# Kernel tuning notes

Hardware: AMD Instinct MI355X
Metric: run time of the kernel (lower is better)

The kernel has to match this reference:

```python
import jax, jax.numpy as jnp
import numpy as np

DIM, DFF, NH = 768, 2048, 12
HD = DIM // NH
N, NOBJ, L = 16, 52, 24
EPS = 1e-5


def setup_inputs() -> dict:
    key = jax.random.key(0)
    ks = jax.random.split(key, 16)
    g = lambda k, shape: jax.random.normal(k, shape, jnp.float32) * 0.02
    inp = {
        "lang": jax.random.normal(ks[0], (N, L, DIM), jnp.float32),
        "obj": jax.random.normal(ks[1], (N, NOBJ, DIM), jnp.float32),
        "lang_mask": jnp.ones((N, L), jnp.int32),
        "obj_mask": jnp.ones((N, NOBJ), jnp.int32),
        "co_mask": jnp.ones((N, L, NOBJ), jnp.int32),
    }
    # two multi-head attention blocks (edge / node): q,k,v,o projections
    for i, nm in enumerate(["e_wq", "e_wk", "e_wv", "e_wo", "n_wq", "n_wk", "n_wv", "n_wo"]):
        inp[nm] = g(ks[2 + i], (DIM, DIM))
        inp[nm.replace("w", "b")] = jnp.zeros((DIM,), jnp.float32)
    inp["ffn_w1"] = g(ks[10], (2 * DIM, DFF)); inp["ffn_b1"] = jnp.zeros((DFF,), jnp.float32)
    inp["ffn_w2"] = g(ks[11], (DFF, DIM)); inp["ffn_b2"] = jnp.zeros((DIM,), jnp.float32)
    for nm in ["ln_e", "ln_q", "ln2"]:
        inp[nm + "_g"] = jnp.ones((DIM,), jnp.float32)
        inp[nm + "_b"] = jnp.zeros((DIM,), jnp.float32)
    return inp


def _layernorm(x, g, b):
    m = jnp.mean(x, -1, keepdims=True)
    v = jnp.mean((x - m) ** 2, -1, keepdims=True)
    return (x - m) * jax.lax.rsqrt(v + EPS) * g + b


def _fwd(lang, obj, co_mask,
         e_wq, e_bq, e_wk, e_bk, e_wv, e_bv, e_wo, e_bo,
         n_wq, n_bq, n_wk, n_bk, n_wv, n_bv, n_wo, n_bo,
         ffn_w1, ffn_b1, ffn_w2, ffn_b2,
         ln_e_g, ln_e_b, ln_q_g, ln_q_b, ln2_g, ln2_b):
    scale = jnp.float32(1.0 / np.sqrt(HD))
    co_t = co_mask.swapaxes(1, 2)  # [N, nobj, L]: query objects attend over lang keys

    # ---- node branch: standard cross-attention obj -> lang ----
    qh = (obj @ n_wq + n_bq).reshape(N, NOBJ, NH, HD)
    kh = (lang @ n_wk + n_bk).reshape(N, L, NH, HD)
    vh = (lang @ n_wv + n_bv).reshape(N, L, NH, HD)
    s = jnp.einsum('nqhd,nlhd->nhql', qh, kh) * scale  # [N,H,nobj,L]
    s = jnp.where(co_t[:, None, :, :] > 0, s, jnp.float32(-1e9))
    a = jax.nn.softmax(s, axis=-1)
    node = jnp.einsum('nhql,nlhd->nqhd', a, vh).reshape(N, NOBJ, DIM) @ n_wo + n_bo

    # ---- edge branch: pairwise diffs attend over lang, then max over partner ----
    diff = obj[:, :, None, :] - obj[:, None, :, :]            # [N,i,j,D]
    qhe = (diff @ e_wq + e_bq).reshape(N, NOBJ, NOBJ, NH, HD)
    khe = (lang @ e_wk + e_bk).reshape(N, L, NH, HD)
    vhe = (lang @ e_wv + e_bv).reshape(N, L, NH, HD)
    se = jnp.einsum('nijhd,nlhd->nhijl', qhe, khe) * scale    # [N,H,i,j,L]
    # mask depends on (n, j, l): torch repeats co_mask^T over the i batch dim
    se = jnp.where(co_t[:, None, None, :, :] > 0, se, jnp.float32(-1e9))
    ae = jax.nn.softmax(se, axis=-1)
    oe = jnp.einsum('nhijl,nlhd->nijhd', ae, vhe).reshape(N, NOBJ, NOBJ, DIM)
    oe = oe @ e_wo + e_bo                                      # [N,i,j,D]
    edge = jnp.max(oe, axis=2)                                 # max over query/partner j -> [N,i,D]

    # ---- fuse ----
    xe = _layernorm(obj + edge, ln_e_g, ln_e_b)
    xn = _layernorm(obj + node, ln_q_g, ln_q_b)
    h = jnp.concatenate((xn, xe), -1)
    h = jax.nn.relu(h @ ffn_w1 + ffn_b1) @ ffn_w2 + ffn_b2
    return _layernorm(xn + h, ln2_g, ln2_b)


def reference(lang, obj, lang_mask, obj_mask, co_mask,
              e_wq, e_bq, e_wk, e_bk, e_wv, e_bv, e_wo, e_bo,
              n_wq, n_bq, n_wk, n_bk, n_wv, n_bv, n_wo, n_bo,
              ffn_w1, ffn_b1, ffn_w2, ffn_b2,
              ln_e_g, ln_e_b, ln_q_g, ln_q_b, ln2_g, ln2_b):
    return _fwd(lang, obj, co_mask,
                e_wq, e_bq, e_wk, e_bk, e_wv, e_bv, e_wo, e_bo,
                n_wq, n_bq, n_wk, n_bk, n_wv, n_bv, n_wo, n_bo,
                ffn_w1, ffn_b1, ffn_w2, ffn_b2,
                ln_e_g, ln_e_b, ln_q_g, ln_q_b, ln2_g, ln2_b)
```

## Files before the change

kernel.cpp:

```cpp
#include <hip/hip_runtime.h>
#include <math.h>

#define NOBJ 52
#define LL 24
#define NHEAD 12

typedef __attribute__((ext_vector_type(8))) short bf16x8;
typedef __attribute__((ext_vector_type(4))) float f32x4;
typedef __attribute__((ext_vector_type(4))) unsigned int u32x4;
typedef __attribute__((ext_vector_type(2))) unsigned int u32x2;

__device__ __forceinline__ unsigned short f2b(float x) {
    union { float f; unsigned int u; } v; v.f = x;
    unsigned int r = v.u + 0x7fffu + ((v.u >> 16) & 1u);
    return (unsigned short)(r >> 16);
}
__device__ __forceinline__ float b2f(unsigned short u) {
    union { unsigned int u; float f; } v; v.u = ((unsigned int)u) << 16;
    return v.f;
}
__device__ __forceinline__ unsigned int pack2(float a, float b) {
    return (unsigned int)f2b(a) | ((unsigned int)f2b(b) << 16);
}
__device__ __forceinline__ f32x4 mfma16(bf16x8 a, bf16x8 b, f32x4 c) {
    return __builtin_amdgcn_mfma_f32_16x16x32_bf16(a, b, c, 0, 0, 0);
}
__device__ __forceinline__ void gl_lds16(const void* g, void* lds) {
    __builtin_amdgcn_global_load_lds(
        (const __attribute__((address_space(1))) unsigned int*)g,
        (__attribute__((address_space(3))) unsigned int*)lds, 16, 0, 0);
}

__device__ __forceinline__ void transpose_tile(const float* __restrict__ src,
    unsigned short* __restrict__ dst, int K, int N, int t, char* smem)
{
    float (*ts)[65] = (float(*)[65])smem;
    const int tid = threadIdx.x;
    const int ntk = K >> 6;
    const int k0 = (t % ntk) << 6, n0 = (t / ntk) << 6;
    const int tx = tid & 63, ty = tid >> 6;
    #pragma unroll
    for (int i2 = 0; i2 < 16; ++i2) {
        const int row = i2 * 4 + ty;
        ts[row][tx] = src[(size_t)(k0 + row) * N + n0 + tx];
    }
    __syncthreads();
    #pragma unroll
    for (int i2 = 0; i2 < 16; ++i2) {
        const int row = i2 * 4 + ty;
        dst[(size_t)(n0 + row) * K + k0 + tx] = f2b(ts[tx][row]);
    }
}

__global__ __launch_bounds__(256)
void pack1_kernel(const float* s0, const float* s1, const float* s2,
                  const float* s3, const float* s4, const float* s5,
                  const float* s6, const float* s7,
                  unsigned short* d0, unsigned short* d1, unsigned short* d2,
                  unsigned short* d3, unsigned short* d4, unsigned short* d5,
                  unsigned short* d6, unsigned short* d7,
                  const float* obj, const float* lang, const float* n_bq,
                  const float* e_bk, const float* e_bv,
                  const float* n_bk, const float* n_bv,
                  unsigned short* objb, unsigned short* langb,
                  float* bqc, float* blc)
{
    __shared__ __align__(16) char smem[16640];
    const int bid = blockIdx.x;
    const int tid = threadIdx.x;
    if (bid < 1152) {
        const int job = bid / 144, t = bid % 144;
        const float* src; unsigned short* dst;
        switch (job) {
            case 0: src = s0; dst = d0; break;
            case 1: src = s1; dst = d1; break;
            case 2: src = s2; dst = d2; break;
            case 3: src = s3; dst = d3; break;
            case 4: src = s4; dst = d4; break;
            case 5: src = s5; dst = d5; break;
            case 6: src = s6; dst = d6; break;
            default: src = s7; dst = d7; break;
        }
        transpose_tile(src, dst, 768, 768, t, smem);
    } else {
        const int base = ((bid - 1152) * 256 + tid) * 4;
        const int T0 = 638976, T1 = 933888, T2 = 935424, T3 = 938496;
        if (base >= T3) return;
        if (base < T0) {
            f32x4 v = *(const f32x4*)(obj + base);
            *(u32x2*)(objb + base) = (u32x2){pack2(v[0], v[1]), pack2(v[2], v[3])};
        } else if (base < T1) {
            const int j = base - T0;
            f32x4 v = *(const f32x4*)(lang + j);
            *(u32x2*)(langb + j) = (u32x2){pack2(v[0], v[1]), pack2(v[2], v[3])};
        } else if (base < T2) {
            const int j = base - T1;
            if (j < 768) { *(f32x4*)(bqc + j) = (f32x4){0.f, 0.f, 0.f, 0.f}; }
            else         { *(f32x4*)(bqc + j) = *(const f32x4*)(n_bq + j - 768); }
        } else {
            const int j = base - T2;
            const int s = j / 768, c = j % 768;
            const float* p = (s == 0) ? e_bk : (s == 1) ? e_bv : (s == 2) ? n_bk : n_bv;
            *(f32x4*)(blc + j) = *(const f32x4*)(p + c);
        }
    }
}

struct GemmJob {
    const unsigned short* A; const unsigned short* Bt; const float* bias;
    float* C; unsigned short* Cb;
    int lda, ldb, ldc, K, nbx, nb, relu, swz;
};

__device__ __forceinline__ void gemm_body(const GemmJob J, int bid, char* smem)
{
    unsigned short* As = (unsigned short*)smem;
    unsigned short* Bs = (unsigned short*)(smem + 16384);
    int bx, by;
    if (J.swz) {
        const int cpx = J.nb >> 3;
        const int gid = (bid & 7) * cpx + (bid >> 3);
        const int nbm = J.nb / J.nbx;
        bx = gid / nbm; by = gid % nbm;
    } else { bx = bid % J.nbx; by = bid / J.nbx; }
    const int n0 = bx * 128, m0 = by * 64;
    const int tid = threadIdx.x;
    const int lane = tid & 63;
    const int w = tid >> 6, wr = w >> 1, wc = w & 1;
    const int lr = lane & 15, lk = lane >> 4;
    const int lda = J.lda, ldb = J.ldb, K = J.K;
    const unsigned short* Ab = J.A + (size_t)m0 * lda;
    const unsigned short* Bb = J.Bt + (size_t)n0 * ldb;

    f32x4 acc[2][4] = {};
    const int NT = K >> 6;

    #pragma unroll
    for (int q = 0; q < 2; ++q) {
        const int c = q * 256 + tid, row = c >> 3, p = (c & 7) ^ (row & 7);
        gl_lds16(Ab + (size_t)row * lda + p * 8, As + c * 8);
    }
    #pragma unroll
    for (int q = 0; q < 4; ++q) {
        const int c = q * 256 + tid, row = c >> 3, p = (c & 7) ^ (row & 7);
        gl_lds16(Bb + (size_t)row * ldb + p * 8, Bs + c * 8);
    }
    __syncthreads();

    for (int t = 0; t < NT; ++t) {
        const int cur = t & 1;
        if (t + 1 < NT) {
            const int k0 = (t + 1) << 6;
            #pragma unroll
            for (int q = 0; q < 2; ++q) {
                const int c = q * 256 + tid, row = c >> 3, p = (c & 7) ^ (row & 7);
                gl_lds16(Ab + (size_t)row * lda + k0 + p * 8, As + (cur ^ 1) * 4096 + c * 8);
            }
            #pragma unroll
            for (int q = 0; q < 4; ++q) {
                const int c = q * 256 + tid, row = c >> 3, p = (c & 7) ^ (row & 7);
                gl_lds16(Bb + (size_t)row * ldb + k0 + p * 8, Bs + (cur ^ 1) * 8192 + c * 8);
            }
        }
        #pragma unroll
        for (int kk = 0; kk < 2; ++kk) {
            bf16x8 af[2], bv[4];
            #pragma unroll
            for (int mt = 0; mt < 2; ++mt) {
                const int row = wr * 32 + mt * 16 + lr;
                const int pc = (kk * 4 + lk) ^ (row & 7);
                af[mt] = *(const bf16x8*)(As + cur * 4096 + row * 64 + pc * 8);
            }
            #pragma unroll
            for (int nt = 0; nt < 4; ++nt) {
                const int col = wc * 64 + nt * 16 + lr;
                const int pc = (kk * 4 + lk) ^ (col & 7);
                bv[nt] = *(const bf16x8*)(Bs + cur * 8192 + col * 64 + pc * 8);
            }
            #pragma unroll
            for (int mt = 0; mt < 2; ++mt)
                #pragma unroll
                for (int nt = 0; nt < 4; ++nt)
                    acc[mt][nt] = mfma16(af[mt], bv[nt], acc[mt][nt]);
        }
        __syncthreads();
    }

    #pragma unroll
    for (int mt = 0; mt < 2; ++mt) {
        #pragma unroll
        for (int nt = 0; nt < 4; ++nt) {
            const int col = n0 + wc * 64 + nt * 16 + lr;
            const float bvv = J.bias ? J.bias[col] : 0.f;
            #pragma unroll
            for (int r = 0; r < 4; ++r) {
                const int row = m0 + wr * 32 + mt * 16 + lk * 4 + r;
                float v = acc[mt][nt][r] + bvv;
                if (J.relu) v = fmaxf(v, 0.f);
                if (J.C)  J.C[(size_t)row * J.ldc + col] = v;
                if (J.Cb) J.Cb[(size_t)row * J.ldc + col] = f2b(v);
            }
        }
    }
}

__global__ __launch_bounds__(256)
void gemm_tn4(GemmJob j0, GemmJob j1, GemmJob j2, GemmJob j3)
{
    __shared__ __align__(16) char smem[49152];
    int bid = blockIdx.x;
    if (bid < j0.nb) { gemm_body(j0, bid, smem); return; }
    bid -= j0.nb;
    if (bid < j1.nb) { gemm_body(j1, bid, smem); return; }
    bid -= j1.nb;
    if (bid < j2.nb) { gemm_body(j2, bid, smem); return; }
    bid -= j2.nb;
    gemm_body(j3, bid, smem);
}

__global__ __launch_bounds__(256)
void proj_pack_kernel(GemmJob j0, GemmJob j1,
                      const float* w1, const float* w2,
                      unsigned short* W1t, unsigned short* W2t)
{
    __shared__ __align__(16) char smem[49152];
    int bid = blockIdx.x;
    if (bid < j0.nb) { gemm_body(j0, bid, smem); return; }
    bid -= j0.nb;
    if (bid < j1.nb) { gemm_body(j1, bid, smem); return; }
    const int t = bid - j1.nb;
    if (t < 768) transpose_tile(w1, W1t, 1536, 2048, t, smem);
    else transpose_tile(w2, W2t, 2048, 768, t - 768, smem);
}

__global__ __launch_bounds__(256)
void mid3_kernel(const unsigned short* __restrict__ QCb,
                 const unsigned short* __restrict__ LCb,
                 const unsigned short* __restrict__ Wet,
                 const unsigned short* __restrict__ Wot,
                 const float* __restrict__ e_bq,
                 unsigned short* __restrict__ VWe,
                 unsigned short* __restrict__ VWn,
                 float* __restrict__ S2e, float* __restrict__ Tb,
                 float* __restrict__ S2n)
{
    __shared__ __align__(16) union USm {
        struct { unsigned short As[8192], Bs[8192]; } g;
        unsigned short Ct[128 * 136];
        struct { float sA[52][65], sB[24][65]; } s;
    } U;
    const int bid = blockIdx.x;
    const int tid = threadIdx.x;

    if (bid < 432) {
        const int sub = bid >= 216;
        const int b = sub ? bid - 216 : bid;
        const int aoff = sub ? 2304 : 768;
        const unsigned short* Bt = sub ? Wot : Wet;
        unsigned short* Vout = sub ? VWn : VWe;

        const int h = b / 18, rm = b % 18, mt = rm / 6, ntile = rm % 6;
        const int m0 = mt * 128, n0 = ntile * 128;
        const int lane = tid & 63, w = tid >> 6, wr = w >> 1, wc = w & 1;
        const int lr = lane & 15, lk = lane >> 4;
        #pragma unroll
        for (int q = 0; q < 4; ++q) {
            const int c = q * 256 + tid, row = c >> 3, p = (c & 7) ^ (row & 7);
            gl_lds16(LCb + (size_t)(m0 + row) * 3072 + aoff + h * 64 + p * 8, &U.g.As[c * 8]);
            gl_lds16(Bt + (size_t)(n0 + row) * 768 + h * 64 + p * 8, &U.g.Bs[c * 8]);
        }
        __syncthreads();
        f32x4 acc[4][4] = {};
        #pragma unroll
        for (int kk = 0; kk < 2; ++kk) {
            bf16x8 af[4], bv[4];
            #pragma unroll
            for (int m2 = 0; m2 < 4; ++m2) {
                const int row = wr * 64 + m2 * 16 + lr;
                const int pc = (kk * 4 + lk) ^ (row & 7);
                af[m2] = *(const bf16x8*)&U.g.As[row * 64 + pc * 8];
            }
            #pragma unroll
            for (int n2 = 0; n2 < 4; ++n2) {
                const int col = wc * 64 + n2 * 16 + lr;
                const int pc = (kk * 4 + lk) ^ (col & 7);
                bv[n2] = *(const bf16x8*)&U.g.Bs[col * 64 + pc * 8];
            }
            #pragma unroll
            for (int m2 = 0; m2 < 4; ++m2)
                #pragma unroll
                for (int n2 = 0; n2 < 4; ++n2)
                    acc[m2][n2] = mfma16(af[m2], bv[n2], acc[m2][n2]);
        }
        __syncthreads();
        #pragma unroll
        for (int m2 = 0; m2 < 4; ++m2)
            #pragma unroll
            for (int n2 = 0; n2 < 4; ++n2) {
                const int col = wc * 64 + n2 * 16 + lr;
                #pragma unroll
                for (int r = 0; r < 4; ++r) {
                    const int row = wr * 64 + m2 * 16 + lk * 4 + r;
                    U.Ct[row * 136 + col] = f2b(acc[m2][n2][r]);
                }
            }
        __syncthreads();
        #pragma unroll
        for (int q = 0; q < 8; ++q) {
            const int item = q * 256 + tid;
            const int dl = item & 127, kg = item >> 7;
            const int m = m0 + kg * 8;
            const int nn = m / 24, l0 = m % 24;
            const int kc = (h * 24 + l0) >> 3;
            const int ks = kc >> 2;
            const int dg = n0 + dl;
            const int kpos = (kc & 3) ^ ((dg >> 1) & 3);
            u32x4 uu;
            #pragma unroll
            for (int e = 0; e < 4; ++e)
                uu[e] = (unsigned int)U.Ct[(kg * 8 + 2 * e) * 136 + dl]
                      | ((unsigned int)U.Ct[(kg * 8 + 2 * e + 1) * 136 + dl] << 16);
            *(u32x4*)(Vout + (size_t)nn * 221184 + ks * 24576 + dg * 32 + kpos * 8) = uu;
        }
    } else {
        const int sub = bid >= 624;
        const int b = bid - (sub ? 624 : 432);
        const int n = b / NHEAD, h = b % NHEAD;
        const int qoff = sub ? 768 : 0, koff = sub ? 1536 : 0;
        float* Sout = sub ? S2n : S2e;
        for (int p = tid; p < 52 * 64; p += 256) {
            const int q = p >> 6, d = p & 63;
            U.s.sA[q][d] = b2f(QCb[(size_t)(n * 52 + q) * 1536 + qoff + h * 64 + d]);
        }
        for (int p = tid; p < 24 * 64; p += 256) {
            const int l = p >> 6, d = p & 63;
            U.s.sB[l][d] = b2f(LCb[(size_t)(n * 24 + l) * 3072 + koff + h * 64 + d]);
        }
        __syncthreads();
        for (int p = tid; p < 52 * 24; p += 256) {
            const int l = p / 52, q = p % 52;
            float s = 0.f;
            #pragma unroll
            for (int d = 0; d < 64; ++d) s += U.s.sA[q][d] * U.s.sB[l][d];
            Sout[((size_t)(n * NHEAD + h) * 24 + l) * 52 + q] = s;
        }
        if (!sub && tid < 24) {
            float s = 0.f;
            #pragma unroll
            for (int d = 0; d < 64; ++d) s += e_bq[h * 64 + d] * U.s.sB[tid][d];
            Tb[((size_t)n * NHEAD + h) * 24 + tid] = s;
        }
    }
}

__global__ __launch_bounds__(512)
void attn_kernel(const float* __restrict__ S2e, const float* __restrict__ Tb,
                 const float* __restrict__ S2n, const int* __restrict__ co_mask,
                 const unsigned short* __restrict__ VWe,
                 const unsigned short* __restrict__ VWn,
                 const float* __restrict__ ebo, const float* __restrict__ nbo,
                 unsigned short* __restrict__ EdgeBb,
                 unsigned short* __restrict__ NodePb)
{
    __shared__ __align__(16) char smem[126464];
    unsigned short* Pf = (unsigned short*)smem;
    unsigned short* Bs = (unsigned short*)(smem + 73728);
    float* SiT = (float*)(smem + 122880);
    unsigned char* cmb = (unsigned char*)(smem + 125184);
    const int bid = blockIdx.x;
    const int tid = threadIdx.x;
    const int lane = tid & 63, w = tid >> 6;
    const int lr = lane & 15, lk = lane >> 4;

    if (bid < 832) {
        const int sw = (bid & 7) * 104 + (bid >> 3);
        const int n = sw / 52;
        const int r52 = sw % 52;
        const int ip = r52 >> 1, dh = r52 & 1;
        const int i0 = ip * 2;
        const unsigned short* Bsrc = VWe + (size_t)n * 221184 + dh * 12288;
        const float* S2x = S2e + (size_t)n * NHEAD * 24 * 52;

        #pragma unroll
        for (int q = 0; q < 3; ++q) {
            const int c = q * 512 + tid;
            gl_lds16(Bsrc + c * 8, Bs + c * 8);
        }
        for (int p = tid; p < 576; p += 512) {
            const int ii = p >= 288 ? 1 : 0;
            const int rl = p - ii * 288;
            SiT[ii * 288 + rl] = S2x[(size_t)rl * 52 + i0 + ii]
                               + Tb[(size_t)n * 288 + rl];
        }
        for (int p = tid; p < 1248; p += 512)
            cmb[p] = (unsigned char)(co_mask[(size_t)n * 1248 + p] > 0);
        __syncthreads();

        for (int p = tid; p < 1248; p += 512) {
            const int ii = p >= 624 ? 1 : 0;
            const int rl = p - ii * 624;
            const int h = rl / 52, j = rl % 52;
            const float* Sc = S2x + (size_t)h * 1248 + j;
            const float* st = SiT + ii * 288 + h * 24;
            float x[24]; float mx = -1e30f;
            #pragma unroll
            for (int l = 0; l < 24; ++l) {
                float v = (st[l] - Sc[l * 52]) * 0.125f;
                v = cmb[l * 52 + j] ? v : -1e9f;
                x[l] = v; mx = fmaxf(mx, v);
            }
            float sum = 0.f;
            #pragma unroll
            for (int l = 0; l < 24; ++l) { const float e = __expf(x[l] - mx); x[l] = e; sum += e; }
            const float inv = 1.f / sum;
            unsigned short* Prow = Pf + ii * 18432 + j * 288;
            const int swk = (j >> 1) & 3;
            #pragma unroll
            for (int c = 0; c < 3; ++c) {
                u32x4 u;
                #pragma unroll
                for (int m = 0; m < 4; ++m)
                    u[m] = pack2(x[c * 8 + 2 * m] * inv, x[c * 8 + 2 * m + 1] * inv);
                *(u32x4*)(Prow + (((3 * h + c) ^ swk) << 3)) = u;
            }
        }
        __syncthreads();

        const int iw = w >> 2, cg = (w & 3) * 96;
        f32x4 acc[4][6] = {};
        for (int ks = 0; ks < 9; ++ks) {
            const int cur = ks & 1;
            if (ks < 8) {
                const unsigned short* src = Bsrc + (size_t)(ks + 1) * 24576;
                #pragma unroll
                for (int q = 0; q < 3; ++q) {
                    const int c = q * 512 + tid;
                    gl_lds16(src + c * 8, Bs + (cur ^ 1) * 12288 + c * 8);
                }
            }
            bf16x8 af[4];
            #pragma unroll
            for (int mt = 0; mt < 4; ++mt) {
                const int row = mt * 16 + lr;
                af[mt] = *(const bf16x8*)(Pf + iw * 18432 + row * 288
                                          + (((ks * 4 + lk) ^ ((row >> 1) & 3)) << 3));
            }
            #pragma unroll
            for (int nt = 0; nt < 6; ++nt) {
                const int cl = cg + nt * 16 + lr;
                bf16x8 bv = *(const bf16x8*)(Bs + cur * 12288 + cl * 32
                                             + ((lk ^ ((cl >> 1) & 3)) << 3));
                #pragma unroll
                for (int mt = 0; mt < 4; ++mt)
                    acc[mt][nt] = mfma16(af[mt], bv, acc[mt][nt]);
            }
            __syncthreads();
        }

        #pragma unroll
        for (int nt = 0; nt < 6; ++nt) {
            float m = -1e30f;
            #pragma unroll
            for (int mt = 0; mt < 4; ++mt)
                #pragma unroll
                for (int r = 0; r < 4; ++r) {
                    const int row = mt * 16 + lk * 4 + r;
                    if (row < NOBJ) m = fmaxf(m, acc[mt][nt][r]);
                }
            m = fmaxf(m, __shfl_xor(m, 16));
            m = fmaxf(m, __shfl_xor(m, 32));
            if (lk == 0) {
                const int col = dh * 384 + cg + nt * 16 + lr;
                EdgeBb[(size_t)(n * 52 + i0 + iw) * 768 + col] = f2b(m + ebo[col]);
            }
        }
    } else {
        const int t = bid - 832;
        const int n = t >> 1, dh = t & 1;
        const unsigned short* Bsrc = VWn + (size_t)n * 221184 + dh * 12288;
        const float* S2x = S2n + (size_t)n * NHEAD * 24 * 52;

        #pragma unroll
        for (int q = 0; q < 3; ++q) {
            const int c = q * 512 + tid;
            gl_lds16(Bsrc + c * 8, Bs + c * 8);
        }
        for (int p = tid; p < 1248; p += 512)
            cmb[p] = (unsigned char)(co_mask[(size_t)n * 1248 + p] > 0);
        __syncthreads();

        for (int p = tid; p < 624; p += 512) {
            const int h = p / 52, q = p % 52;
            const float* Sc = S2x + (size_t)h * 1248 + q;
            float x[24]; float mx = -1e30f;
            #pragma unroll
            for (int l = 0; l < 24; ++l) {
                float v = Sc[l * 52] * 0.125f;
                v = cmb[l * 52 + q] ? v : -1e9f;
                x[l] = v; mx = fmaxf(mx, v);
            }
            float sum = 0.f;
            #pragma unroll
            for (int l = 0; l < 24; ++l) { const float e = __expf(x[l] - mx); x[l] = e; sum += e; }
            const float inv = 1.f / sum;
            unsigned short* Prow = Pf + q * 288;
            const int swk = (q >> 1) & 3;
            #pragma unroll
            for (int c = 0; c < 3; ++c) {
                u32x4 u;
                #pragma unroll
                for (int m = 0; m < 4; ++m)
                    u[m] = pack2(x[c * 8 + 2 * m] * inv, x[c * 8 + 2 * m + 1] * inv);
                *(u32x4*)(Prow + (((3 * h + c) ^ swk) << 3)) = u;
            }
        }
        __syncthreads();

        const int cg = w * 48;
        f32x4 acc[4][3] = {};
        for (int ks = 0; ks < 9; ++ks) {
            const int cur = ks & 1;
            if (ks < 8) {
                const unsigned short* src = Bsrc + (size_t)(ks + 1) * 24576;
                #pragma unroll
                for (int q = 0; q < 3; ++q) {
                    const int c = q * 512 + tid;
                    gl_lds16(src + c * 8, Bs + (cur ^ 1) * 12288 + c * 8);
                }
            }
            bf16x8 af[4];
            #pragma unroll
            for (int mt = 0; mt < 4; ++mt) {
                const int row = mt * 16 + lr;
                af[mt] = *(const bf16x8*)(Pf + row * 288
                                          + (((ks * 4 + lk) ^ ((row >> 1) & 3)) << 3));
            }
            #pragma unroll
            for (int nt = 0; nt < 3; ++nt) {
                const int cl = cg + nt * 16 + lr;
                bf16x8 bv = *(const bf16x8*)(Bs + cur * 12288 + cl * 32
                                             + ((lk ^ ((cl >> 1) & 3)) << 3));
                #pragma unroll
                for (int mt = 0; mt < 4; ++mt)
                    acc[mt][nt] = mfma16(af[mt], bv, acc[mt][nt]);
            }
            __syncthreads();
        }

        #pragma unroll
        for (int nt = 0; nt < 3; ++nt) {
            const int col = dh * 384 + cg + nt * 16 + lr;
            const float bv = nbo[col];
            #pragma unroll
            for (int mt = 0; mt < 4; ++mt)
                #pragma unroll
                for (int r = 0; r < 4; ++r) {
                    const int row = mt * 16 + lk * 4 + r;
                    if (row < NOBJ)
                        NodePb[(size_t)(n * 52 + row) * 768 + col] = f2b(acc[mt][nt][r] + bv);
                }
        }
    }
}

__global__ __launch_bounds__(256)
void ln_dual_kernel(const float* __restrict__ obj,
                    const unsigned short* __restrict__ NodePb,
                    const unsigned short* __restrict__ EdgeBb,
                    const float* __restrict__ gq, const float* __restrict__ bq,
                    const float* __restrict__ ge, const float* __restrict__ be,
                    unsigned short* __restrict__ Fusedb)
{
    __shared__ float red[8];
    const int job = blockIdx.x >= 832;
    const int row = blockIdx.x - (job ? 832 : 0);
    const int tid = threadIdx.x;
    const unsigned short* x2 = (job ? EdgeBb : NodePb) + (size_t)row * 768;
    const float* x1 = obj + (size_t)row * 768;
    const float* g = job ? ge : gq;
    const float* bb = job ? be : bq;
    float v[3]; float s = 0.f;
    #pragma unroll
    for (int c = 0; c < 3; ++c) {
        const int col = tid + 256 * c;
        v[c] = x1[col] + b2f(x2[col]); s += v[c];
    }
    #pragma unroll
    for (int o = 32; o; o >>= 1) s += __shfl_xor(s, o);
    if ((tid & 63) == 0) red[tid >> 6] = s;
    __syncthreads();
    const float mean = (red[0] + red[1] + red[2] + red[3]) * (1.f / 768.f);
    float var = 0.f;
    #pragma unroll
    for (int c = 0; c < 3; ++c) { const float d = v[c] - mean; var += d * d; }
    #pragma unroll
    for (int o = 32; o; o >>= 1) var += __shfl_xor(var, o);
    __syncthreads();
    if ((tid & 63) == 0) red[4 + (tid >> 6)] = var;
    __syncthreads();
    const float vt = (red[4] + red[5] + red[6] + red[7]) * (1.f / 768.f);
    const float rs = rsqrtf(vt + 1e-5f);
    unsigned short* dst = Fusedb + (size_t)row * 1536 + (job ? 768 : 0);
    #pragma unroll
    for (int c = 0; c < 3; ++c) {
        const int col = tid + 256 * c;
        dst[col] = f2b((v[c] - mean) * rs * g[col] + bb[col]);
    }
}

__global__ __launch_bounds__(256)
void ln2_kernel(const unsigned short* __restrict__ x1b,
                const float* __restrict__ Hp, const float* __restrict__ b2,
                const float* __restrict__ g, const float* __restrict__ bb,
                float* __restrict__ dst)
{
    __shared__ float red[8];
    const int row = blockIdx.x, tid = threadIdx.x;
    float v[3]; float s = 0.f;
    #pragma unroll
    for (int c = 0; c < 3; ++c) {
        const int col = tid + 256 * c;
        const size_t o = (size_t)row * 768 + col;
        float h = Hp[o] + Hp[638976 + o] + Hp[2 * 638976 + o] + Hp[3 * 638976 + o];
        v[c] = b2f(x1b[(size_t)row * 1536 + col]) + h + b2[col];
        s += v[c];
    }
    #pragma unroll
    for (int o = 32; o; o >>= 1) s += __shfl_xor(s, o);
    if ((tid & 63) == 0) red[tid >> 6] = s;
    __syncthreads();
    const float mean = (red[0] + red[1] + red[2] + red[3]) * (1.f / 768.f);
    float var = 0.f;
    #pragma unroll
    for (int c = 0; c < 3; ++c) { const float d = v[c] - mean; var += d * d; }
    #pragma unroll
    for (int o = 32; o; o >>= 1) var += __shfl_xor(var, o);
    __syncthreads();
    if ((tid & 63) == 0) red[4 + (tid >> 6)] = var;
    __syncthreads();
    const float vt = (red[4] + red[5] + red[6] + red[7]) * (1.f / 768.f);
    const float rs = rsqrtf(vt + 1e-5f);
    #pragma unroll
    for (int c = 0; c < 3; ++c) {
        const int col = tid + 256 * c;
        dst[(size_t)row * 768 + col] = (v[c] - mean) * rs * g[col] + bb[col];
    }
}

extern "C" void kernel_launch(void* const* d_in, const int* in_sizes, int n_in,
                              void* d_out, int out_size, void* d_ws, size_t ws_size,
                              hipStream_t stream)
{
    (void)in_sizes; (void)n_in; (void)out_size; (void)ws_size;
    const float* lang  = (const float*)d_in[0];
    const float* obj   = (const float*)d_in[1];
    const int* co_mask = (const int*)d_in[4];
    const float* e_wq = (const float*)d_in[5];
    const float* e_bq = (const float*)d_in[6];
    const float* e_wk = (const float*)d_in[7];
    const float* e_bk = (const float*)d_in[8];
    const float* e_wv = (const float*)d_in[9];
    const float* e_bv = (const float*)d_in[10];
    const float* e_wo = (const float*)d_in[11];
    const float* e_bo = (const float*)d_in[12];
    const float* n_wq = (const float*)d_in[13];
    const float* n_bq = (const float*)d_in[14];
    const float* n_wk = (const float*)d_in[15];
    const float* n_bk = (const float*)d_in[16];
    const float* n_wv = (const float*)d_in[17];
    const float* n_bv = (const float*)d_in[18];
    const float* n_wo = (const float*)d_in[19];
    const float* n_bo = (const float*)d_in[20];
    const float* ffn_w1 = (const float*)d_in[21];
    const float* ffn_b1 = (const float*)d_in[22];
    const float* ffn_w2 = (const float*)d_in[23];
    const float* ffn_b2 = (const float*)d_in[24];
    const float* ln_e_g = (const float*)d_in[25];
    const float* ln_e_b = (const float*)d_in[26];
    const float* ln_q_g = (const float*)d_in[27];
    const float* ln_q_b = (const float*)d_in[28];
    const float* ln2_g = (const float*)d_in[29];
    const float* ln2_b = (const float*)d_in[30];
    float* out = (float*)d_out;

    char* wsb = (char*)d_ws;
    unsigned short* Wqt   = (unsigned short*)(wsb + 0);
    unsigned short* Wlt   = (unsigned short*)(wsb + 2359296);
    unsigned short* Wet   = (unsigned short*)(wsb + 7077888);
    unsigned short* Wot   = (unsigned short*)(wsb + 8257536);
    unsigned short* W1t   = (unsigned short*)(wsb + 9437184);
    unsigned short* W2t   = (unsigned short*)(wsb + 15728640);
    unsigned short* objb  = (unsigned short*)(wsb + 18874368);
    unsigned short* langb = (unsigned short*)(wsb + 20152320);
    float*          bqc   = (float*)(wsb + 20742144);
    float*          blc   = (float*)(wsb + 20748288);
    unsigned short* QCb   = (unsigned short*)(wsb + 20760576);
    unsigned short* LCb   = (unsigned short*)(wsb + 23316480);
    float*          S2e   = (float*)(wsb + 25675776);
    float*          Tb    = (float*)(wsb + 26634240);
    float*          S2n   = (float*)(wsb + 26652672);
    unsigned short* VWe   = (unsigned short*)(wsb + 27611136);
    unsigned short* VWn   = (unsigned short*)(wsb + 34689024);
    unsigned short* NodePb= (unsigned short*)(wsb + 41766912);
    unsigned short* EdgeBb= (unsigned short*)(wsb + 43044864);
    unsigned short* Fusedb= (unsigned short*)(wsb + 44322816);
    unsigned short* H1b   = (unsigned short*)(wsb + 46878720);
    float*          Hp    = (float*)(wsb + 50286592);

    dim3 blk(256);
    pack1_kernel<<<2069, blk, 0, stream>>>(
        e_wq, n_wq, e_wk, e_wv, n_wk, n_wv, n_wo, e_wo,
        Wqt, Wqt + 589824, Wlt, Wlt + 589824, Wlt + 2 * 589824, Wlt + 3 * 589824,
        Wot, Wet,
        obj, lang, n_bq, e_bk, e_bv, n_bk, n_bv, objb, langb, bqc, blc);
    {
        GemmJob p0 = {objb, Wqt, bqc, nullptr, QCb, 768, 768, 1536, 768, 12, 156, 0, 0};
        GemmJob p1 = {langb, Wlt, blc, nullptr, LCb, 768, 768, 3072, 768, 24, 144, 0, 0};
        proj_pack_kernel<<<1452, blk, 0, stream>>>(p0, p1, ffn_w1, ffn_w2, W1t, W2t);
    }
    mid3_kernel<<<816, blk, 0, stream>>>(QCb, LCb, Wet, Wot, e_bq,
                                         VWe, VWn, S2e, Tb, S2n);
    attn_kernel<<<864, dim3(512), 0, stream>>>(S2e, Tb, S2n, co_mask, VWe, VWn,
                                               e_bo, n_bo, EdgeBb, NodePb);
    ln_dual_kernel<<<1664, blk, 0, stream>>>(obj, NodePb, EdgeBb, ln_q_g, ln_q_b,
                                             ln_e_g, ln_e_b, Fusedb);
    {
        GemmJob p0 = {Fusedb, W1t, ffn_b1, nullptr, H1b, 1536, 1536, 2048, 1536, 16, 208, 1, 1};
        gemm_tn4<<<208, blk, 0, stream>>>(p0, p0, p0, p0);
    }
    {
        GemmJob q0 = {H1b,        W2t,        nullptr, Hp,               nullptr, 2048, 2048, 768, 512, 6, 78, 0, 0};
        GemmJob q1 = {H1b + 512,  W2t + 512,  nullptr, Hp + 638976,      nullptr, 2048, 2048, 768, 512, 6, 78, 0, 0};
        GemmJob q2 = {H1b + 1024, W2t + 1024, nullptr, Hp + 2 * 638976,  nullptr, 2048, 2048, 768, 512, 6, 78, 0, 0};
        GemmJob q3 = {H1b + 1536, W2t + 1536, nullptr, Hp + 3 * 638976,  nullptr, 2048, 2048, 768, 512, 6, 78, 0, 0};
        gemm_tn4<<<312, blk, 0, stream>>>(q0, q1, q2, q3);
    }
    ln2_kernel<<<832, blk, 0, stream>>>(Fusedb, Hp, ffn_b2, ln2_g, ln2_b, out);
}
```

Measured before the change: 129.6 us.

## Triple-buffer B tiles in attention GEMM with vmcnt waits and single barrier

Moves the V·Wo B-operand staging in both edge and node branches from double to triple buffering, prefetching two k-steps ahead. Each iteration now waits with an explicit vmcnt on outstanding async loads and uses one s_barrier in place of the trailing __syncthreads. MFMA sections are wrapped in setprio to favour compute waves. The goal is to hide global-to-LDS latency behind MFMA work, at the cost of about 24KB more LDS and reliance on correct hand-written vmcnt counts.

```diff
diff --git a/kernel.cpp b/kernel.cpp
--- a/kernel.cpp
+++ b/kernel.cpp
@@ -362,11 +362,11 @@
                  unsigned short* __restrict__ EdgeBb,
                  unsigned short* __restrict__ NodePb)
 {
-    __shared__ __align__(16) char smem[126464];
+    __shared__ __align__(16) char smem[151040];
     unsigned short* Pf = (unsigned short*)smem;
     unsigned short* Bs = (unsigned short*)(smem + 73728);
-    float* SiT = (float*)(smem + 122880);
-    unsigned char* cmb = (unsigned char*)(smem + 125184);
+    float* SiT = (float*)(smem + 147456);
+    unsigned char* cmb = (unsigned char*)(smem + 149760);
     const int bid = blockIdx.x;
     const int tid = threadIdx.x;
     const int lane = tid & 63, w = tid >> 6;
@@ -382,9 +382,14 @@
         const float* S2x = S2e + (size_t)n * NHEAD * 24 * 52;
 
         #pragma unroll
-        for (int q = 0; q < 3; ++q) {
-            const int c = q * 512 + tid;
-            gl_lds16(Bsrc + c * 8, Bs + c * 8);
+        for (int s = 0; s < 2; ++s) {
+            const unsigned short* src = Bsrc + (size_t)s * 24576;
+            unsigned short* dstb = Bs + s * 12288;
+            #pragma unroll
+            for (int q = 0; q < 3; ++q) {
+                const int c = q * 512 + tid;
+                gl_lds16(src + c * 8, dstb + c * 8);
+            }
         }
         for (int p = tid; p < 576; p += 512) {
             const int ii = p >= 288 ? 1 : 0;
@@ -429,15 +434,21 @@
         const int iw = w >> 2, cg = (w & 3) * 96;
         f32x4 acc[4][6] = {};
         for (int ks = 0; ks < 9; ++ks) {
-            const int cur = ks & 1;
-            if (ks < 8) {
-                const unsigned short* src = Bsrc + (size_t)(ks + 1) * 24576;
+            if (ks < 8) { asm volatile("s_waitcnt vmcnt(3)" ::: "memory"); }
+            else        { asm volatile("s_waitcnt vmcnt(0)" ::: "memory"); }
+            __builtin_amdgcn_sched_barrier(0);
+            __builtin_amdgcn_s_barrier();
+            __builtin_amdgcn_sched_barrier(0);
+            if (ks + 2 <= 8) {
+                const unsigned short* src = Bsrc + (size_t)(ks + 2) * 24576;
+                unsigned short* dstb = Bs + ((ks + 2) % 3) * 12288;
                 #pragma unroll
                 for (int q = 0; q < 3; ++q) {
                     const int c = q * 512 + tid;
-                    gl_lds16(src + c * 8, Bs + (cur ^ 1) * 12288 + c * 8);
+                    gl_lds16(src + c * 8, dstb + c * 8);
                 }
             }
+            const unsigned short* Bcur = Bs + (ks % 3) * 12288;
             bf16x8 af[4];
             #pragma unroll
             for (int mt = 0; mt < 4; ++mt) {
@@ -445,16 +456,17 @@
                 af[mt] = *(const bf16x8*)(Pf + iw * 18432 + row * 288
                                           + (((ks * 4 + lk) ^ ((row >> 1) & 3)) << 3));
             }
+            __builtin_amdgcn_s_setprio(1);
             #pragma unroll
             for (int nt = 0; nt < 6; ++nt) {
                 const int cl = cg + nt * 16 + lr;
-                bf16x8 bv = *(const bf16x8*)(Bs + cur * 12288 + cl * 32
+                bf16x8 bv = *(const bf16x8*)(Bcur + cl * 32
                                              + ((lk ^ ((cl >> 1) & 3)) << 3));
                 #pragma unroll
                 for (int mt = 0; mt < 4; ++mt)
                     acc[mt][nt] = mfma16(af[mt], bv, acc[mt][nt]);
             }
-            __syncthreads();
+            __builtin_amdgcn_s_setprio(0);
         }
 
         #pragma unroll
@@ -481,9 +493,14 @@
         const float* S2x = S2n + (size_t)n * NHEAD * 24 * 52;
 
         #pragma unroll
-        for (int q = 0; q < 3; ++q) {
-            const int c = q * 512 + tid;
-            gl_lds16(Bsrc + c * 8, Bs + c * 8);
+        for (int s = 0; s < 2; ++s) {
+            const unsigned short* src = Bsrc + (size_t)s * 24576;
+            unsigned short* dstb = Bs + s * 12288;
+            #pragma unroll
+            for (int q = 0; q < 3; ++q) {
+                const int c = q * 512 + tid;
+                gl_lds16(src + c * 8, dstb + c * 8);
+            }
         }
         for (int p = tid; p < 1248; p += 512)
             cmb[p] = (unsigned char)(co_mask[(size_t)n * 1248 + p] > 0);
@@ -519,15 +536,21 @@
         const int cg = w * 48;
         f32x4 acc[4][3] = {};
         for (int ks = 0; ks < 9; ++ks) {
-            const int cur = ks & 1;
-            if (ks < 8) {
-                const unsigned short* src = Bsrc + (size_t)(ks + 1) * 24576;
+            if (ks < 8) { asm volatile("s_waitcnt vmcnt(3)" ::: "memory"); }
+            else        { asm volatile("s_waitcnt vmcnt(0)" ::: "memory"); }
+            __builtin_amdgcn_sched_barrier(0);
+            __builtin_amdgcn_s_barrier();
+            __builtin_amdgcn_sched_barrier(0);
+            if (ks + 2 <= 8) {
+                const unsigned short* src = Bsrc + (size_t)(ks + 2) * 24576;
+                unsigned short* dstb = Bs + ((ks + 2) % 3) * 12288;
                 #pragma unroll
                 for (int q = 0; q < 3; ++q) {
                     const int c = q * 512 + tid;
-                    gl_lds16(src + c * 8, Bs + (cur ^ 1) * 12288 + c * 8);
+                    gl_lds16(src + c * 8, dstb + c * 8);
                 }
             }
+            const unsigned short* Bcur = Bs + (ks % 3) * 12288;
             bf16x8 af[4];
             #pragma unroll
             for (int mt = 0; mt < 4; ++mt) {
@@ -535,16 +558,17 @@
                 af[mt] = *(const bf16x8*)(Pf + row * 288
                                           + (((ks * 4 + lk) ^ ((row >> 1) & 3)) << 3));
             }
+            __builtin_amdgcn_s_setprio(1);
             #pragma unroll
             for (int nt = 0; nt < 3; ++nt) {
                 const int cl = cg + nt * 16 + lr;
-                bf16x8 bv = *(const bf16x8*)(Bs + cur * 12288 + cl * 32
+                bf16x8 bv = *(const bf16x8*)(Bcur + cl * 32
                                              + ((lk ^ ((cl >> 1) & 3)) << 3));
                 #pragma unroll
                 for (int mt = 0; mt < 4; ++mt)
                     acc[mt][nt] = mfma16(af[mt], bv, acc[mt][nt]);
             }
-            __syncthreads();
+            __builtin_amdgcn_s_setprio(0);
         }
 
         #pragma unroll
```

Result: no change. 132.0 us (+1.9%).
